# Performance work log

Measured on AMD Instinct MI355X. Metric: run time of the kernel, lower is better.

The kernel has to match this reference:

```python
import jax, jax.numpy as jnp
import numpy as np
import math

B, S, V, D = 512, 256, 100000, 64
KS = [7, 5]
NF = [8, 16]
K_TOP = 4
NCLS = 6
ROWS = [D, D // 2, D // 4]  # [64, 32, 16]


def setup_inputs() -> dict:
    key = jax.random.key(0)
    ks = jax.random.split(key, 6)
    x = jax.random.randint(ks[0], (B, S), 0, V)
    emb = jax.random.normal(ks[1], (V, D), jnp.float32) * 0.1
    # conv1: in=1*64, out=8*64=512, groups=64 -> weight (512, 1, 7)
    w1 = jax.random.normal(ks[2], (NF[0] * ROWS[0], 1, KS[0]), jnp.float32) * 0.1
    b1 = jnp.zeros((NF[0] * ROWS[0],), jnp.float32)
    # conv2: in=8*32=256, out=16*32=512, groups=32 -> weight (512, 8, 5)
    w2 = jax.random.normal(ks[3], (NF[1] * ROWS[1], NF[0], KS[1]), jnp.float32) * 0.05
    b2 = jnp.zeros((NF[1] * ROWS[1],), jnp.float32)
    fc_in = ROWS[2] * NF[1] * K_TOP  # 16*16*4 = 1024
    fc_w = jax.random.normal(ks[4], (NCLS, fc_in), jnp.float32) * 0.05
    fc_b = jnp.zeros((NCLS,), jnp.float32)
    return dict(x=x, emb=emb, w1=w1, b1=b1, w2=w2, b2=b2, fc_w=fc_w, fc_b=fc_b)


def _kmax_ordered(h, k):
    # order-preserving k-max pooling along last axis
    _, idx = jax.lax.top_k(h, k)
    idx = jnp.sort(idx, axis=-1)
    return jnp.take_along_axis(h, idx, axis=-1)


def _forward(x, emb, w1, b1, w2, b2, fc_w, fc_b):
    h = emb[x].transpose(0, 2, 1)  # (B, D, S)
    ws, bs = (w1, w2), (b1, b2)
    L = len(KS)
    for i in range(L):
        K = KS[i]
        nf = NF[i]
        groups = ROWS[i]
        # wide grouped conv1d, padding = K-1 both sides -> out_len = S + K - 1
        h = jax.lax.conv_general_dilated(
            h, ws[i], window_strides=(1,), padding=[(K - 1, K - 1)],
            dimension_numbers=('NCH', 'OIH', 'NCH'), feature_group_count=groups,
        ) + bs[i][None, :, None]
        b_, d_, s_ = h.shape
        # to_channel_view: (b, d, s) -> (b, nf, d//nf, s)
        h = h.reshape(b_, d_ // nf, nf, s_).transpose(0, 2, 1, 3)
        # Fold(2,2): sum adjacent row pairs along the row axis
        h = h.reshape(b_, nf, (d_ // nf) // 2, 2, s_).sum(axis=3)
        # from_channel_view: (b, nf, rows, s) -> (b, rows*nf, s)
        h = h.transpose(0, 2, 1, 3).reshape(b_, -1, s_)
        # dynamic k-max pool (last layer uses fixed k_top)
        if i == L - 1:
            k = K_TOP
        else:
            k = max(K_TOP, math.ceil((L - (i + 1)) / L * h.shape[-1]))
        h = _kmax_ordered(h, k)
        h = jnp.tanh(h)
    # dropout is identity in eval mode
    h = h.reshape(h.shape[0], -1)  # (B, rows[-1]*nf[-1]*k_top) = (B, 1024)
    return h @ fc_w.T + fc_b


def reference(x, emb, w1, b1, w2, b2, fc_w, fc_b):
    return _forward(x, emb, w1, b1, w2, b2, fc_w, fc_b)
```

## Files before the change

kernel.cpp:

```cpp
#include <hip/hip_runtime.h>
#include <stdint.h>

#define S_LEN 256
#define OUT1  262
#define K1SEL 131
#define OUT2  135
#define W1T_OFF 0
#define W2T_OFF 3584
#define B1C_OFF 24064
#define B2C_OFF 24320
#define WREG    1120

typedef float v2f __attribute__((ext_vector_type(2)));
__device__ __forceinline__ v2f fma2(v2f a, v2f b, v2f c) {
    return __builtin_elementwise_fma(a, b, c);
}

__device__ __forceinline__ int lane_prefix(unsigned long long m) {
    return __builtin_amdgcn_mbcnt_hi((uint32_t)(m >> 32),
           __builtin_amdgcn_mbcnt_lo((uint32_t)m, 0));
}
__device__ __forceinline__ uint32_t f2ord(float x) {
    uint32_t b = __float_as_uint(x);
    return (b & 0x80000000u) ? ~b : (b | 0x80000000u);
}
__device__ __forceinline__ float ord2f(uint32_t s) {
    uint32_t b = (s & 0x80000000u) ? (s & 0x7FFFFFFFu) : ~s;
    return __uint_as_float(b);
}
__device__ __forceinline__ float fast_tanh(float x) {
    float e = __expf(2.0f * x);
    return (e - 1.0f) * __builtin_amdgcn_rcpf(e + 1.0f);
}
typedef unsigned long long u64;
__device__ __forceinline__ u64 shflx64(u64 v, int m) {
    uint32_t lo = (uint32_t)__shfl_xor((int)(uint32_t)v, m, 64);
    uint32_t hi = (uint32_t)__shfl_xor((int)(uint32_t)(v >> 32), m, 64);
    return ((u64)hi << 32) | lo;
}
__device__ __forceinline__ u64 maxu64(u64 a, u64 b) { return a > b ? a : b; }
__device__ __forceinline__ u64 minu64(u64 a, u64 b) { return a < b ? a : b; }

extern "C" __global__ void dcnn_prep(const float* __restrict__ w1, const float* __restrict__ b1,
                                     const float* __restrict__ w2, const float* __restrict__ b2,
                                     const float* __restrict__ fcb, float* __restrict__ out,
                                     float* __restrict__ ws) {
    int i = blockIdx.x * 256 + threadIdx.x;
    if (i < 3072) out[i] = fcb[i % 6];
    if (i < W2T_OFF) {
        int d = i / 56, r = i % 56, k = r / 8, f = r % 8;
        ws[i] = w1[(d * 8 + f) * 7 + k];
    } else if (i < B1C_OFF) {
        int q = i - W2T_OFF;
        int g = q / 640, r = q % 640;
        int ic = r / 80, r2 = r % 80;
        int k = r2 / 16, f2 = r2 % 16;
        ws[i] = w2[((g * 16 + f2) * 8 + ic) * 5 + k];
    } else if (i < B2C_OFF) {
        int q = i - B1C_OFF;
        int r2 = q / 8, f = q % 8;
        ws[i] = b1[(2 * r2) * 8 + f] + b1[(2 * r2 + 1) * 8 + f];
    } else {
        int q = i - B2C_OFF;
        int r3 = q / 16, f2 = q % 16;
        ws[i] = b2[(2 * r3) * 16 + f2] + b2[(2 * r3 + 1) * 16 + f2];
    }
}

extern "C" __global__
__attribute__((amdgpu_flat_work_group_size(256, 256), amdgpu_waves_per_eu(4, 8)))
void dcnn_main(const int* __restrict__ x, const float* __restrict__ emb,
               const float* __restrict__ fcw, const float* __restrict__ ws,
               float* __restrict__ out) {
    __shared__ float uni[4 * WREG];
    __shared__ int   xs[S_LEN];
    __shared__ float p2loc[128];
    __shared__ float fred[4][3];

    const int tid    = threadIdx.x;
    const int lane   = tid & 63;
    const int wv     = __builtin_amdgcn_readfirstlane(tid >> 6);
    const int sample = blockIdx.x >> 3;
    const int q8     = blockIdx.x & 7;
    const int sl     = q8 * 2 + (wv >> 1);
    const int rs     = wv & 1;

    const float* w1t = ws + W1T_OFF;
    const float* w2t = ws + W2T_OFF;
    const float* b1c = ws + B1C_OFF;
    const float* b2c = ws + B2C_OFF;

    xs[tid] = x[sample * S_LEN + tid];
    __syncthreads();

    float*  reg   = uni + wv * WREG;
    float2* rowsW = (float2*)reg;
    float*  p1w   = reg;

    if (lane < 8) {
        rowsW[lane]       = make_float2(0.f, 0.f);
        rowsW[264 + lane] = make_float2(0.f, 0.f);
    }
    const int dbase = 4 * sl + 2 * rs;
#pragma unroll
    for (int m = 0; m < 4; ++m) {
        int j  = lane + 64 * m;
        int xi = xs[j];
        rowsW[8 + j] = *(const float2*)(emb + (size_t)xi * 64 + dbase);
    }

    v2f acc2[4][5];
#pragma unroll
    for (int j = 0; j < 4; ++j) {
        v2f bz = *(const v2f*)(b1c + (2 * sl + rs) * 8 + 2 * j);
#pragma unroll
        for (int m = 0; m < 5; ++m) acc2[j][m] = bz;
    }
    int tA[5];
#pragma unroll
    for (int m = 0; m < 5; ++m) { int t = lane + 64 * m; tA[m] = (t < OUT1) ? t : (OUT1 - 1); }

#pragma unroll 1
    for (int k = 0; k < 7; ++k) {
        v2f wa[4], wb[4];
#pragma unroll
        for (int j = 0; j < 4; ++j) {
            wa[j] = *(const v2f*)(w1t + (dbase * 7 + k) * 8 + 2 * j);
            wb[j] = *(const v2f*)(w1t + ((dbase + 1) * 7 + k) * 8 + 2 * j);
        }
#pragma unroll
        for (int m = 0; m < 5; ++m) {
            float2 v = rowsW[tA[m] + 2 + k];
            v2f vx = { v.x, v.x };
            v2f vy = { v.y, v.y };
#pragma unroll
            for (int j = 0; j < 4; ++j) {
                acc2[j][m] = fma2(wa[j], vx, acc2[j][m]);
                acc2[j][m] = fma2(wb[j], vy, acc2[j][m]);
            }
        }
    }

    {
        int c = lane >> 3, j = lane & 7;
        int pos = (j < 4) ? j : (131 + j);
        p1w[c * 140 + pos] = 0.f;
    }

    uint32_t uu[4][2][5];
#pragma unroll
    for (int cp = 0; cp < 4; ++cp) {
#pragma unroll
        for (int m = 0; m < 4; ++m) {
            uu[cp][0][m] = f2ord(acc2[cp][m].x);
            uu[cp][1][m] = f2ord(acc2[cp][m].y);
        }
        uu[cp][0][4] = (lane < 6) ? f2ord(acc2[cp][4].x) : 0u;
        uu[cp][1][4] = (lane < 6) ? f2ord(acc2[cp][4].y) : 0u;
    }
    uint32_t pre[8];
    int ge[8];
#pragma unroll
    for (int c = 0; c < 8; ++c) { pre[c] = 0u; ge[c] = 0x7FFFFFFF; }
#pragma unroll 1
    for (int bit = 31; bit >= 16; --bit) {
#pragma unroll
        for (int c = 0; c < 8; ++c) {
            uint32_t cand = pre[c] | (1u << bit);
            int n = 0;
#pragma unroll
            for (int m = 0; m < 5; ++m)
                n += __popcll(__ballot(uu[c >> 1][c & 1][m] >= cand));
            if (n >= K1SEL) { pre[c] = cand; ge[c] = n; }
        }
    }
#pragma unroll
    for (int cp = 0; cp < 4; ++cp) {
        uint32_t preA = pre[2 * cp], preB = pre[2 * cp + 1];
        float* dstA = p1w + (2 * cp) * 140 + 4;
        float* dstB = p1w + (2 * cp + 1) * 140 + 4;
        if (ge[2 * cp] == K1SEL && ge[2 * cp + 1] == K1SEL) {
            int kpA = 0, kpB = 0;
#pragma unroll
            for (int m = 0; m < 5; ++m) {
                unsigned long long kmA = __ballot(uu[cp][0][m] >= preA);
                unsigned long long kmB = __ballot(uu[cp][1][m] >= preB);
                int posA = kpA + lane_prefix(kmA);
                int posB = kpB + lane_prefix(kmB);
                if (uu[cp][0][m] >= preA) dstA[posA] = ord2f(uu[cp][0][m]);
                if (uu[cp][1][m] >= preB) dstB[posB] = ord2f(uu[cp][1][m]);
                kpA += __popcll(kmA); kpB += __popcll(kmB);
            }
        } else {
#pragma unroll 1
            for (int bit = 15; bit >= 0; --bit) {
                uint32_t cA = preA | (1u << bit);
                uint32_t cB = preB | (1u << bit);
                int na = 0, nb = 0;
#pragma unroll
                for (int m = 0; m < 5; ++m) {
                    na += __popcll(__ballot(uu[cp][0][m] >= cA));
                    nb += __popcll(__ballot(uu[cp][1][m] >= cB));
                }
                if (na >= K1SEL) preA = cA;
                if (nb >= K1SEL) preB = cB;
            }
            int cgtA = 0, cgtB = 0;
#pragma unroll
            for (int m = 0; m < 5; ++m) {
                cgtA += __popcll(__ballot(uu[cp][0][m] > preA));
                cgtB += __popcll(__ballot(uu[cp][1][m] > preB));
            }
            const int needA = K1SEL - cgtA;
            const int needB = K1SEL - cgtB;
            int eqA = 0, kpA = 0, eqB = 0, kpB = 0;
#pragma unroll
            for (int m = 0; m < 5; ++m) {
                unsigned long long emA = __ballot(uu[cp][0][m] == preA);
                unsigned long long emB = __ballot(uu[cp][1][m] == preB);
                int erA = eqA + lane_prefix(emA);
                int erB = eqB + lane_prefix(emB);
                bool keepA = (uu[cp][0][m] > preA) || ((uu[cp][0][m] == preA) && (erA < needA));
                bool keepB = (uu[cp][1][m] > preB) || ((uu[cp][1][m] == preB) && (erB < needB));
                unsigned long long kmA = __ballot(keepA);
                unsigned long long kmB = __ballot(keepB);
                int posA = kpA + lane_prefix(kmA);
                int posB = kpB + lane_prefix(kmB);
                if (keepA) dstA[posA] = ord2f(uu[cp][0][m]);
                if (keepB) dstB[posB] = ord2f(uu[cp][1][m]);
                eqA += __popcll(emA); kpA += __popcll(kmA);
                eqB += __popcll(emB); kpB += __popcll(kmB);
            }
        }
    }

#pragma unroll
    for (int i = 0; i < 17; ++i) {
        int idx = lane + 64 * i;
        p1w[idx] = fast_tanh(p1w[idx]);
    }
    if (lane < 32) {
        int idx = lane + 64 * 17;
        p1w[idx] = fast_tanh(p1w[idx]);
    }

    const int g = 2 * sl + rs;
    const v2f* b2v = (const v2f*)(b2c + sl * 16);
    v2f a2v[8][2];
#pragma unroll
    for (int j = 0; j < 8; ++j) {
        v2f bz = rs ? (v2f){0.f, 0.f} : b2v[j];
        a2v[j][0] = bz; a2v[j][1] = bz;
    }

#pragma unroll 1
    for (int ic = 0; ic < 8; ++ic) {
        const float* src = p1w + ic * 140;
        float win[2][5];
#pragma unroll
        for (int m = 0; m < 2; ++m) {
#pragma unroll
            for (int k = 0; k < 5; ++k) win[m][k] = src[lane + 64 * m + k];
        }
#pragma unroll
        for (int k = 0; k < 5; ++k) {
            const v2f* wv2 = (const v2f*)(w2t + ((g * 8 + ic) * 5 + k) * 16);
            v2f s0 = { win[0][k], win[0][k] };
            v2f s1 = { win[1][k], win[1][k] };
#pragma unroll
            for (int j = 0; j < 8; ++j) {
                v2f w = wv2[j];
                a2v[j][0] = fma2(w, s0, a2v[j][0]);
                a2v[j][1] = fma2(w, s1, a2v[j][1]);
            }
        }
    }

    const int tt = lane >> 3;
    const int tj = lane & 7;
    v2f at = (!rs) ? b2v[tj] : (v2f){0.f, 0.f};
    {
        const float* tsrc0 = p1w + 128 + tt;
        const float* tw    = w2t + g * 640 + 2 * tj;
#pragma unroll
        for (int ic = 0; ic < 8; ++ic) {
#pragma unroll
            for (int k = 0; k < 5; ++k) {
                float sv = tsrc0[ic * 140 + k];
                v2f w = *(const v2f*)(tw + (ic * 5 + k) * 16);
                v2f sb = { sv, sv };
                at = fma2(w, sb, at);
            }
        }
    }

    float* scr = uni + (wv & ~1) * WREG;
    __syncthreads();
    if (rs) {
#pragma unroll
        for (int j = 0; j < 8; ++j) {
            scr[(2 * j) * 137 + lane]           = a2v[j][0].x;
            scr[(2 * j + 1) * 137 + lane]       = a2v[j][0].y;
            scr[(2 * j) * 137 + lane + 64]      = a2v[j][1].x;
            scr[(2 * j + 1) * 137 + lane + 64]  = a2v[j][1].y;
        }
        if (lane < 56) {
            scr[(2 * tj) * 137 + 128 + tt]     = at.x;
            scr[(2 * tj + 1) * 137 + 128 + tt] = at.y;
        }
    }
    __syncthreads();
    if (!rs) {
#pragma unroll
        for (int j = 0; j < 8; ++j) {
            scr[(2 * j) * 137 + lane]           += a2v[j][0].x;
            scr[(2 * j + 1) * 137 + lane]       += a2v[j][0].y;
            scr[(2 * j) * 137 + lane + 64]      += a2v[j][1].x;
            scr[(2 * j + 1) * 137 + lane + 64]  += a2v[j][1].y;
        }
        if (lane < 56) {
            scr[(2 * tj) * 137 + 128 + tt]     += at.x;
            scr[(2 * tj + 1) * 137 + 128 + tt] += at.y;
        }
    }
    __syncthreads();

    {
        const int f2o = (lane >> 3) + 8 * rs;
        const int seg = lane & 7;
        const int tstart = seg * 17;
        const int tend = (seg == 7) ? (OUT2 - 119) : 17;
        const float* src = scr + f2o * 137 + tstart;
        const uint32_t tb = 0xFFFFFFFFu - (uint32_t)tstart;
        u64 L0 = 0, L1 = 0, L2 = 0, L3 = 0;
#pragma unroll 1
        for (int i = 0; i < 17; ++i) {
            float v = src[(i < tend) ? i : 0];
            u64 kk = ((u64)f2ord(v) << 32) | (u64)(tb - (uint32_t)i);
            if (i >= tend) kk = 0;
            bool b0 = kk > L0, b1 = kk > L1, b2 = kk > L2, b3 = kk > L3;
            L3 = b3 ? (b2 ? L2 : kk) : L3;
            L2 = b2 ? (b1 ? L1 : kk) : L2;
            L1 = b1 ? (b0 ? L0 : kk) : L1;
            L0 = b0 ? kk : L0;
        }
#pragma unroll
        for (int d = 1; d <= 4; d <<= 1) {
            u64 M0 = shflx64(L0, d), M1 = shflx64(L1, d);
            u64 M2 = shflx64(L2, d), M3 = shflx64(L3, d);
            u64 r0 = maxu64(L0, M0);
            u64 r1 = minu64(maxu64(L0, M1), maxu64(L1, M0));
            u64 r2 = minu64(minu64(maxu64(L0, M2), maxu64(L1, M1)), maxu64(L2, M0));
            u64 r3k = minu64(minu64(maxu64(L0, M3), maxu64(L1, M2)),
                             minu64(maxu64(L2, M1), maxu64(L3, M0)));
            L0 = r0; L1 = r1; L2 = r2; L3 = r3k;
        }
        if (seg == 0) {
#define CSW2(a, bb) { if ((uint32_t)(bb) > (uint32_t)(a)) { u64 tt2 = (a); (a) = (bb); (bb) = tt2; } }
            CSW2(L0, L1); CSW2(L2, L3); CSW2(L0, L2); CSW2(L1, L3); CSW2(L1, L2);
#undef CSW2
            float* qp = &p2loc[(wv >> 1) * 64 + f2o * 4];
            qp[0] = ord2f((uint32_t)(L0 >> 32));
            qp[1] = ord2f((uint32_t)(L1 >> 32));
            qp[2] = ord2f((uint32_t)(L2 >> 32));
            qp[3] = ord2f((uint32_t)(L3 >> 32));
        }
    }
    __syncthreads();

    {
        const int nb = (wv >> 1) * 3;
        const int fh = (wv & 1) * 64;
        float pv = fast_tanh(p2loc[fh + lane]);
#pragma unroll
        for (int i = 0; i < 3; ++i) {
            float s = pv * fcw[(nb + i) * 1024 + q8 * 128 + fh + lane];
#pragma unroll
            for (int off = 32; off > 0; off >>= 1) s += __shfl_xor(s, off, 64);
            if (lane == 0) fred[wv][i] = s;
        }
    }
    __syncthreads();
    if (tid < 6) {
        float v = (tid < 3) ? (fred[0][tid] + fred[1][tid])
                            : (fred[2][tid - 3] + fred[3][tid - 3]);
        atomicAdd(&out[sample * 6 + tid], v);
    }
}

extern "C" void kernel_launch(void* const* d_in, const int* in_sizes, int n_in,
                              void* d_out, int out_size, void* d_ws, size_t ws_size,
                              hipStream_t stream) {
    (void)in_sizes; (void)n_in; (void)out_size; (void)ws_size;
    const int*   x   = (const int*)d_in[0];
    const float* emb = (const float*)d_in[1];
    const float* w1  = (const float*)d_in[2];
    const float* b1  = (const float*)d_in[3];
    const float* w2  = (const float*)d_in[4];
    const float* b2  = (const float*)d_in[5];
    const float* fcw = (const float*)d_in[6];
    const float* fcb = (const float*)d_in[7];
    float* outp = (float*)d_out;
    float* wsf  = (float*)d_ws;

    dcnn_prep<<<96, 256, 0, stream>>>(w1, b1, w2, b2, fcb, outp, wsf);
    dcnn_main<<<4096, 256, 0, stream>>>(x, emb, fcw, wsf, outp);
}
```

Baseline: 195.3 us.

## Repartition conv2 work across wave pairs by time half and drop x staging

The conv2 work split changes. Each wave of a pair now computes all input channels from both waves' pooled buffers for one half of the time range, instead of computing half the channels for all times and reducing the partials through shared memory with extra read-modify-write passes. The token indices are read directly from global memory instead of being staged through shared memory behind a barrier. The ordered-key to float conversion moves from the scatter step into the tanh pass, and the per-segment top-4 scan is fully unrolled with a simplified tail mask. The aim is fewer barriers and less shared-memory reduction traffic, at the cost of each wave reading the other wave's data and doing a serial tail computation on one wave.

```diff
diff --git a/kernel.cpp b/kernel.cpp
--- a/kernel.cpp
+++ b/kernel.cpp
@@ -56,7 +56,7 @@
         int ic = r / 80, r2 = r % 80;
         int k = r2 / 16, f2 = r2 % 16;
         ws[i] = w2[((g * 16 + f2) * 8 + ic) * 5 + k];
-    } else if (i < B2C_OFF) {
+    } else if (i < B1C_OFF + 256 && i >= B1C_OFF) {
         int q = i - B1C_OFF;
         int r2 = q / 8, f = q % 8;
         ws[i] = b1[(2 * r2) * 8 + f] + b1[(2 * r2 + 1) * 8 + f];
@@ -73,7 +73,6 @@
                const float* __restrict__ fcw, const float* __restrict__ ws,
                float* __restrict__ out) {
     __shared__ float uni[4 * WREG];
-    __shared__ int   xs[S_LEN];
     __shared__ float p2loc[128];
     __shared__ float fred[4][3];
 
@@ -90,9 +89,6 @@
     const float* b1c = ws + B1C_OFF;
     const float* b2c = ws + B2C_OFF;
 
-    xs[tid] = x[sample * S_LEN + tid];
-    __syncthreads();
-
     float*  reg   = uni + wv * WREG;
     float2* rowsW = (float2*)reg;
     float*  p1w   = reg;
@@ -102,10 +98,11 @@
         rowsW[264 + lane] = make_float2(0.f, 0.f);
     }
     const int dbase = 4 * sl + 2 * rs;
+    const int* xrow = x + sample * S_LEN;
 #pragma unroll
     for (int m = 0; m < 4; ++m) {
         int j  = lane + 64 * m;
-        int xi = xs[j];
+        int xi = xrow[j];
         rowsW[8 + j] = *(const float2*)(emb + (size_t)xi * 64 + dbase);
     }
 
@@ -144,7 +141,7 @@
     {
         int c = lane >> 3, j = lane & 7;
         int pos = (j < 4) ? j : (131 + j);
-        p1w[c * 140 + pos] = 0.f;
+        p1w[c * 140 + pos] = __uint_as_float(0x80000000u);
     }
 
     uint32_t uu[4][2][5];
@@ -187,8 +184,8 @@
                 unsigned long long kmB = __ballot(uu[cp][1][m] >= preB);
                 int posA = kpA + lane_prefix(kmA);
                 int posB = kpB + lane_prefix(kmB);
-                if (uu[cp][0][m] >= preA) dstA[posA] = ord2f(uu[cp][0][m]);
-                if (uu[cp][1][m] >= preB) dstB[posB] = ord2f(uu[cp][1][m]);
+                if (uu[cp][0][m] >= preA) dstA[posA] = __uint_as_float(uu[cp][0][m]);
+                if (uu[cp][1][m] >= preB) dstB[posB] = __uint_as_float(uu[cp][1][m]);
                 kpA += __popcll(kmA); kpB += __popcll(kmB);
             }
         } else {
@@ -226,8 +223,8 @@
                 unsigned long long kmB = __ballot(keepB);
                 int posA = kpA + lane_prefix(kmA);
                 int posB = kpB + lane_prefix(kmB);
-                if (keepA) dstA[posA] = ord2f(uu[cp][0][m]);
-                if (keepB) dstB[posB] = ord2f(uu[cp][1][m]);
+                if (keepA) dstA[posA] = __uint_as_float(uu[cp][0][m]);
+                if (keepB) dstB[posB] = __uint_as_float(uu[cp][1][m]);
                 eqA += __popcll(emA); kpA += __popcll(kmA);
                 eqB += __popcll(emB); kpB += __popcll(kmB);
             }
@@ -237,91 +234,73 @@
 #pragma unroll
     for (int i = 0; i < 17; ++i) {
         int idx = lane + 64 * i;
-        p1w[idx] = fast_tanh(p1w[idx]);
+        p1w[idx] = fast_tanh(ord2f(__float_as_uint(p1w[idx])));
     }
     if (lane < 32) {
         int idx = lane + 64 * 17;
-        p1w[idx] = fast_tanh(p1w[idx]);
-    }
-
-    const int g = 2 * sl + rs;
-    const v2f* b2v = (const v2f*)(b2c + sl * 16);
-    v2f a2v[8][2];
-#pragma unroll
-    for (int j = 0; j < 8; ++j) {
-        v2f bz = rs ? (v2f){0.f, 0.f} : b2v[j];
-        a2v[j][0] = bz; a2v[j][1] = bz;
-    }
-
-#pragma unroll 1
-    for (int ic = 0; ic < 8; ++ic) {
-        const float* src = p1w + ic * 140;
-        float win[2][5];
-#pragma unroll
-        for (int m = 0; m < 2; ++m) {
-#pragma unroll
-            for (int k = 0; k < 5; ++k) win[m][k] = src[lane + 64 * m + k];
-        }
-#pragma unroll
-        for (int k = 0; k < 5; ++k) {
-            const v2f* wv2 = (const v2f*)(w2t + ((g * 8 + ic) * 5 + k) * 16);
-            v2f s0 = { win[0][k], win[0][k] };
-            v2f s1 = { win[1][k], win[1][k] };
-#pragma unroll
-            for (int j = 0; j < 8; ++j) {
-                v2f w = wv2[j];
-                a2v[j][0] = fma2(w, s0, a2v[j][0]);
-                a2v[j][1] = fma2(w, s1, a2v[j][1]);
+        p1w[idx] = fast_tanh(ord2f(__float_as_uint(p1w[idx])));
+    }
+
+    __syncthreads();
+
+    const float* pairp = uni + (wv & ~1) * WREG;
+    const v2f*   b2v   = (const v2f*)(b2c + sl * 16);
+    const int    t0    = rs ? 64 : 0;
+    v2f acc[8];
+#pragma unroll
+    for (int j = 0; j < 8; ++j) acc[j] = b2v[j];
+
+#pragma unroll 1
+    for (int hc = 0; hc < 2; ++hc) {
+        const float* psrc = pairp + hc * WREG;
+        const float* wg   = w2t + (2 * sl + hc) * 640;
+#pragma unroll 1
+        for (int ic = 0; ic < 8; ++ic) {
+            const float* src = psrc + ic * 140 + t0 + lane;
+            float win[5];
+#pragma unroll
+            for (int k = 0; k < 5; ++k) win[k] = src[k];
+#pragma unroll
+            for (int k = 0; k < 5; ++k) {
+                const v2f* wv2 = (const v2f*)(wg + (ic * 5 + k) * 16);
+                v2f s = { win[k], win[k] };
+#pragma unroll
+                for (int j = 0; j < 8; ++j) acc[j] = fma2(wv2[j], s, acc[j]);
             }
         }
     }
 
     const int tt = lane >> 3;
     const int tj = lane & 7;
-    v2f at = (!rs) ? b2v[tj] : (v2f){0.f, 0.f};
-    {
-        const float* tsrc0 = p1w + 128 + tt;
-        const float* tw    = w2t + g * 640 + 2 * tj;
-#pragma unroll
-        for (int ic = 0; ic < 8; ++ic) {
-#pragma unroll
-            for (int k = 0; k < 5; ++k) {
-                float sv = tsrc0[ic * 140 + k];
-                v2f w = *(const v2f*)(tw + (ic * 5 + k) * 16);
-                v2f sb = { sv, sv };
-                at = fma2(w, sb, at);
-            }
-        }
-    }
-
+    v2f at = b2v[tj];
+    if (!rs) {
+#pragma unroll 1
+        for (int hc = 0; hc < 2; ++hc) {
+            const float* tsrc = pairp + hc * WREG + 128 + tt;
+            const float* tw   = w2t + (2 * sl + hc) * 640 + 2 * tj;
+#pragma unroll
+            for (int ic = 0; ic < 8; ++ic) {
+#pragma unroll
+                for (int k = 0; k < 5; ++k) {
+                    float sv = tsrc[ic * 140 + k];
+                    v2f w = *(const v2f*)(tw + (ic * 5 + k) * 16);
+                    v2f sb = { sv, sv };
+                    at = fma2(w, sb, at);
+                }
+            }
+        }
+    }
+
+    __syncthreads();
     float* scr = uni + (wv & ~1) * WREG;
-    __syncthreads();
-    if (rs) {
-#pragma unroll
-        for (int j = 0; j < 8; ++j) {
-            scr[(2 * j) * 137 + lane]           = a2v[j][0].x;
-            scr[(2 * j + 1) * 137 + lane]       = a2v[j][0].y;
-            scr[(2 * j) * 137 + lane + 64]      = a2v[j][1].x;
-            scr[(2 * j + 1) * 137 + lane + 64]  = a2v[j][1].y;
-        }
-        if (lane < 56) {
-            scr[(2 * tj) * 137 + 128 + tt]     = at.x;
-            scr[(2 * tj + 1) * 137 + 128 + tt] = at.y;
-        }
-    }
-    __syncthreads();
-    if (!rs) {
-#pragma unroll
-        for (int j = 0; j < 8; ++j) {
-            scr[(2 * j) * 137 + lane]           += a2v[j][0].x;
-            scr[(2 * j + 1) * 137 + lane]       += a2v[j][0].y;
-            scr[(2 * j) * 137 + lane + 64]      += a2v[j][1].x;
-            scr[(2 * j + 1) * 137 + lane + 64]  += a2v[j][1].y;
-        }
-        if (lane < 56) {
-            scr[(2 * tj) * 137 + 128 + tt]     += at.x;
-            scr[(2 * tj + 1) * 137 + 128 + tt] += at.y;
-        }
+#pragma unroll
+    for (int j = 0; j < 8; ++j) {
+        scr[(2 * j) * 137 + t0 + lane]     = acc[j].x;
+        scr[(2 * j + 1) * 137 + t0 + lane] = acc[j].y;
+    }
+    if (!rs && lane < 56) {
+        scr[(2 * tj) * 137 + 128 + tt]     = at.x;
+        scr[(2 * tj + 1) * 137 + 128 + tt] = at.y;
     }
     __syncthreads();
 
@@ -329,15 +308,14 @@
         const int f2o = (lane >> 3) + 8 * rs;
         const int seg = lane & 7;
         const int tstart = seg * 17;
-        const int tend = (seg == 7) ? (OUT2 - 119) : 17;
         const float* src = scr + f2o * 137 + tstart;
         const uint32_t tb = 0xFFFFFFFFu - (uint32_t)tstart;
         u64 L0 = 0, L1 = 0, L2 = 0, L3 = 0;
-#pragma unroll 1
+#pragma unroll
         for (int i = 0; i < 17; ++i) {
-            float v = src[(i < tend) ? i : 0];
+            float v = src[i];
             u64 kk = ((u64)f2ord(v) << 32) | (u64)(tb - (uint32_t)i);
-            if (i >= tend) kk = 0;
+            if (i == 16 && seg == 7) kk = 0;
             bool b0 = kk > L0, b1 = kk > L1, b2 = kk > L2, b3 = kk > L3;
             L3 = b3 ? (b2 ? L2 : kk) : L3;
             L2 = b2 ? (b1 ? L1 : kk) : L2;
```

Result: slower. 209.3 us (+7.2%).
